# Kernel tuning notes

Hardware: AMD Instinct MI355X
Metric: run time of the kernel (lower is better)

Reference implementation:

```python
import jax, jax.numpy as jnp
import numpy as np

Z_DIM = 32
POLY_ORDER = 3
INCLUDE_BIAS = True

# Static index arrays replicating the nested-loop term ordering of the torch code.
_I2, _J2 = np.triu_indices(Z_DIM)  # pairs (i, j) with i <= j, row-major in i -> matches loop order
_TRIPLES = np.array([(i, j, k) for i in range(Z_DIM) for j in range(i, Z_DIM) for k in range(j, Z_DIM)], dtype=np.int32)
_TI, _TJ, _TK = _TRIPLES[:, 0], _TRIPLES[:, 1], _TRIPLES[:, 2]


def build_library(z):
    # z: [B, d] -> Theta: [B, n_terms], same column order as build_library_torch
    B = z.shape[0]
    terms = []
    if INCLUDE_BIAS:
        terms.append(jnp.ones((B, 1), dtype=z.dtype))
    terms.append(z)
    if POLY_ORDER >= 2:
        terms.append(z[:, _I2] * z[:, _J2])  # [B, C(d+1,2)] quadratic terms
    if POLY_ORDER >= 3:
        terms.append(z[:, _TI] * z[:, _TJ] * z[:, _TK])  # [B, C(d+2,3)] cubic terms
    return jnp.concatenate(terms, axis=1)


def setup_inputs() -> dict:
    key = jax.random.key(0)
    k1, k2 = jax.random.split(key)
    B = 65536
    n_terms = 6545  # 1 + 32 + 528 + 5984 for d=32, order=3, bias
    z = jax.random.normal(k1, (B, Z_DIM), dtype=jnp.float32)
    Xi = jax.random.normal(k2, (n_terms, Z_DIM), dtype=jnp.float32)
    Xi_mask = jnp.ones((n_terms, Z_DIM), dtype=jnp.float32)
    z_mean = jnp.zeros((1, Z_DIM), dtype=jnp.float32)
    z_std = jnp.ones((1, Z_DIM), dtype=jnp.float32)
    return {"z": z, "Xi": Xi, "Xi_mask": Xi_mask, "z_mean": z_mean, "z_std": z_std}


def reference(z, Xi, Xi_mask, z_mean, z_std):
    # NOTE: the original module computes z_norm = (z - z_mean) / z_std but
    # never uses it; Theta is built from the raw z. Reproduce exactly.
    Theta = build_library(z)            # [B, n_terms]
    Xi_eff = Xi * Xi_mask               # [n_terms, z_dim]
    dz_dt = Theta @ Xi_eff              # [B, z_dim]
    return dz_dt
```

## Files before the change

kernel.cpp:

```cpp
#include <hip/hip_runtime.h>


#define Z 32
#define ROWS 65536
#define NTILE (ROWS / 32)
#define NBLK (NTILE / 2)

#define NCHUNK 552
#define NGRAN (NCHUNK * 2)

typedef short short8 __attribute__((ext_vector_type(8)));
typedef float f32x16 __attribute__((ext_vector_type(16)));
typedef float float2v __attribute__((ext_vector_type(2)));

struct Sched {
    int nq[4];
    unsigned long long m2[NCHUNK];
    short rt[NGRAN * 8];
};

constexpr Sched make_sched() {
    Sched s{};
    short gi[NGRAN] = {}, gj[NGRAN] = {};
    char gt[NGRAN] = {}, gq[NGRAN] = {};
    int tidx[32][32] = {}, pidx[32] = {};
    {
        int n = 0;
        for (int a = 0; a < 32; ++a)
            for (int b = a; b < 32; ++b) { tidx[a][b] = n; n += 32 - b; }
        for (int i = 0; i < 32; ++i) pidx[i] = i * 32 - i * (i - 1) / 2;
    }
    int g = 0;
    for (int q = 0; q < 4; ++q) {
        int g0 = g;
        for (int b = 0; b < 32; ++b)
            if ((b >> 3) <= q)
                for (int a = 0; a <= b; ++a) { gi[g]=(short)a; gj[g]=(short)b; gt[g]=0; gq[g]=(char)q; ++g; }
        for (int b = 0; b < 32; ++b)
            if ((b >> 3) >= q) { gi[g]=(short)b; gj[g]=32; gt[g]=1; gq[g]=(char)q; ++g; }
        gi[g]=32; gj[g]=32; gt[g]=2; gq[g]=(char)q; ++g;
        while ((g - g0) & 7) { gi[g]=32; gj[g]=32; gt[g]=3; gq[g]=(char)q; ++g; }
        s.nq[q] = (g - g0) / 2;
    }
    for (int c = 0; c < NCHUNK; ++c) {
        unsigned lo = ((unsigned)gi[2*c]   * 4u) | (((unsigned)gj[2*c]   * 4u) << 16);
        unsigned hi = ((unsigned)gi[2*c+1] * 4u) | (((unsigned)gj[2*c+1] * 4u) << 16);
        s.m2[c] = (unsigned long long)lo | ((unsigned long long)hi << 32);
    }
    for (int gg = 0; gg < NGRAN; ++gg) {
        int i = gi[gg], j = gj[gg], ty = gt[gg], q = gq[gg];
        for (int jj = 0; jj < 8; ++jj) {
            int k = 8 * q + jj, row = -1;
            if (ty == 0)      { if (k >= j) row = 561 + tidx[i][j] + (k - j); }
            else if (ty == 1) { if (k <= i) row = 33 + pidx[k] + (i - k); }
            else if (ty == 2) { row = 1 + k; }
            s.rt[gg * 8 + jj] = (short)row;
        }
    }
    return s;
}
constexpr Sched S = make_sched();
static_assert(S.nq[0] == 36 && S.nq[1] == 84 && S.nq[2] == 160 && S.nq[3] == 272, "chunk counts");

__device__ __forceinline__ unsigned pack_bf16(float s0, float s1) {
#if __has_builtin(__builtin_amdgcn_cvt_pk_bf16_f32)
    return __builtin_bit_cast(unsigned, __builtin_amdgcn_cvt_pk_bf16_f32(s0, s1));
#else
    unsigned b0 = __builtin_bit_cast(unsigned, s0) + 0x8000u;
    unsigned b1 = __builtin_bit_cast(unsigned, s1) + 0x8000u;
    return __builtin_amdgcn_perm(b1, b0, 0x07060302u);
#endif
}

__global__ void sindy_prep(const float* __restrict__ Xi,
                           const float* __restrict__ Xi_mask,
                           uint2* __restrict__ Bp2, size_t ws_size) {
    int tid = blockIdx.x * blockDim.x + threadIdx.x;
    if (tid >= NGRAN * 64) return;
    int g = tid >> 6;
    int lane = tid & 63;
    int n = lane & 31, rep = lane >> 5;
    const short* rt = &S.rt[g * 8 + 4 * rep];
    unsigned v[4];
#pragma unroll
    for (int jj = 0; jj < 4; ++jj) {
        int row = rt[jj];
        float f = 0.0f;
        if (row >= 0) f = Xi[row * Z + n] * Xi_mask[row * Z + n];
        unsigned u = __builtin_bit_cast(unsigned, f);
        v[jj] = (u + 0x7FFFu + ((u >> 16) & 1u)) >> 16;
    }
    int c = g >> 1, h = g & 1;
    size_t idx = ((size_t)c * 64 + h * 32 + n) * 2 + rep;
    if ((idx + 1) * 8 <= ws_size)
        Bp2[idx] = uint2{v[0] | (v[1] << 16), v[2] | (v[3] << 16)};
}

template<int Q>
__device__ __forceinline__ void seg_run(int c0, int nG,
                                        const uint4* __restrict__ bpl,
                                        const float2v (&zr2)[16],
                                        const char* zbase, bool hi, f32x16& acc) {
    const uint4* p = bpl + (size_t)c0 * 64;
    uint4 cur0 = p[0], cur1 = p[64], cur2 = p[128], cur3 = p[192];
    int c = c0;
    auto body = [&](uint4 b0, uint4 b1, uint4 b2, uint4 b3) {
        const uint4 bb[4] = {b0, b1, b2, b3};
#pragma unroll
        for (int i = 0; i < 4; ++i) {
            unsigned long long m2 = S.m2[c + i];
            unsigned mw = hi ? (unsigned)(m2 >> 32) : (unsigned)m2;
            float zi = *(const float*)(zbase + (mw & 0xFFFFu));
            float zj = *(const float*)(zbase + (mw >> 16));
            float pp = zi * zj;
            float2v p2; p2.x = pp; p2.y = pp;
            union { unsigned u[4]; short8 s; } a;
#pragma unroll
            for (int r = 0; r < 4; ++r) {
                float2v t = p2 * zr2[4 * Q + r];
                a.u[r] = pack_bf16(t.x, t.y);
            }
            union { uint4 v; short8 s; } b; b.v = bb[i];
            acc = __builtin_amdgcn_mfma_f32_32x32x16_bf16(a.s, b.s, acc, 0, 0, 0);
        }
        c += 4;
    };
    for (int g = 0; g < nG - 1; ++g) {
        const uint4* pn = p + 256;
        uint4 n0 = pn[0], n1 = pn[64], n2 = pn[128], n3 = pn[192];
        body(cur0, cur1, cur2, cur3);
        cur0 = n0; cur1 = n1; cur2 = n2; cur3 = n3;
        p = pn;
    }
    body(cur0, cur1, cur2, cur3);
}

__global__ __launch_bounds__(256, 4) void sindy_mfma(const float* __restrict__ z,
                                                     const float* __restrict__ Xi,
                                                     const float* __restrict__ Xi_mask,
                                                     const uint4* __restrict__ Bp,
                                                     float* __restrict__ out) {
    const int lane = threadIdx.x & 63;
    const int w = threadIdx.x >> 6;
    const int tib = w >> 1;
    const int kh = w & 1;
    const int m = lane & 31;
    const int half = lane >> 5;
    const int tile = blockIdx.x * 2 + tib;
    const long R = (long)tile * 32;

    __shared__ float zs[2][32][33];
    __shared__ float cs[2][32][32];

    float2v zr2[16];
    const float4* z4 = (const float4*)(z + (R + m) * Z);
#pragma unroll
    for (int t = 0; t < 8; ++t) {
        float4 v = z4[t];
        zr2[2*t]   = float2v{v.x, v.y};
        zr2[2*t+1] = float2v{v.z, v.w};
    }
    if (kh == 0) {
#pragma unroll
        for (int t = 0; t < 8; ++t) {
            zs[tib][m][half * 16 + 2*t]     = zr2[half * 8 + t].x;
            zs[tib][m][half * 16 + 2*t + 1] = zr2[half * 8 + t].y;
        }
        if (half == 0) zs[tib][m][32] = 1.0f;
    }
    __syncthreads();

    f32x16 acc = {};
    const char* zbase = (const char*)&zs[tib][m][0];
    const uint4* bpl = Bp + lane;
    const bool hi = (half != 0);

    if (kh == 0) {
        seg_run<0>(  0,  9, bpl, zr2, zbase, hi, acc);
        seg_run<1>( 36, 21, bpl, zr2, zbase, hi, acc);
        seg_run<2>(120, 40, bpl, zr2, zbase, hi, acc);
    } else {
        seg_run<3>(280, 68, bpl, zr2, zbase, hi, acc);
#pragma unroll
        for (int r = 0; r < 16; ++r) {
            int row = (r & 3) + 8 * (r >> 2) + 4 * half;
            cs[tib][row][m] = acc[r];
        }
    }
    __syncthreads();

    if (kh == 0) {
        const float bias = Xi[m] * Xi_mask[m];
        float* orow = out + R * Z;
#pragma unroll
        for (int r = 0; r < 16; ++r) {
            int row = (r & 3) + 8 * (r >> 2) + 4 * half;
            orow[row * Z + m] = acc[r] + cs[tib][row][m] + bias;
        }
    }
}

extern "C" void kernel_launch(void* const* d_in, const int* in_sizes, int n_in,
                              void* d_out, int out_size, void* d_ws, size_t ws_size,
                              hipStream_t stream) {
    const float* z       = (const float*)d_in[0];
    const float* Xi      = (const float*)d_in[1];
    const float* Xi_mask = (const float*)d_in[2];
    float* out = (float*)d_out;
    uint4* Bp  = (uint4*)d_ws;

    int prep_threads = NGRAN * 64;
    sindy_prep<<<(prep_threads + 255) / 256, 256, 0, stream>>>(Xi, Xi_mask, (uint2*)d_ws, ws_size);
    sindy_mfma<<<NBLK, 256, 0, stream>>>(z, Xi, Xi_mask, Bp, out);
}
```

Measured before the change: 134.0 us.

## Rebalance K split across waves and software-pipeline schedule and z-product loads

Moves one chunk group from the first wave pair to the second so each handles 276 chunks instead of 280/272. The index schedule is copied into shared memory as per-granule words and prefetched two stages ahead. The z_i*z_j products for the next stage are computed before the current MFMAs issue, and the next B fragments are carried across segments instead of being reloaded. z values are now read from shared memory rather than kept as 32 registers, which lowers register pressure but adds LDS reads and a bit more LDS.

```diff
diff --git a/kernel.cpp b/kernel.cpp
--- a/kernel.cpp
+++ b/kernel.cpp
@@ -8,6 +8,7 @@
 
 #define NCHUNK 552
 #define NGRAN (NCHUNK * 2)
+#define KH_SPLIT 276
 
 typedef short short8 __attribute__((ext_vector_type(8)));
 typedef float f32x16 __attribute__((ext_vector_type(16)));
@@ -15,7 +16,7 @@
 
 struct Sched {
     int nq[4];
-    unsigned long long m2[NCHUNK];
+    unsigned mg[NGRAN];
     short rt[NGRAN * 8];
 };
 
@@ -42,12 +43,8 @@
         while ((g - g0) & 7) { gi[g]=32; gj[g]=32; gt[g]=3; gq[g]=(char)q; ++g; }
         s.nq[q] = (g - g0) / 2;
     }
-    for (int c = 0; c < NCHUNK; ++c) {
-        unsigned lo = ((unsigned)gi[2*c]   * 4u) | (((unsigned)gj[2*c]   * 4u) << 16);
-        unsigned hi = ((unsigned)gi[2*c+1] * 4u) | (((unsigned)gj[2*c+1] * 4u) << 16);
-        s.m2[c] = (unsigned long long)lo | ((unsigned long long)hi << 32);
-    }
     for (int gg = 0; gg < NGRAN; ++gg) {
+        s.mg[gg] = ((unsigned)gi[gg] * 4u) | (((unsigned)gj[gg] * 4u) << 16);
         int i = gi[gg], j = gj[gg], ty = gt[gg], q = gq[gg];
         for (int jj = 0; jj < 8; ++jj) {
             int k = 8 * q + jj, row = -1;
@@ -96,43 +93,72 @@
         Bp2[idx] = uint2{v[0] | (v[1] << 16), v[2] | (v[3] << 16)};
 }
 
-template<int Q>
-__device__ __forceinline__ void seg_run(int c0, int nG,
-                                        const uint4* __restrict__ bpl,
-                                        const float2v (&zr2)[16],
-                                        const char* zbase, bool hi, f32x16& acc) {
-    const uint4* p = bpl + (size_t)c0 * 64;
-    uint4 cur0 = p[0], cur1 = p[64], cur2 = p[128], cur3 = p[192];
-    int c = c0;
-    auto body = [&](uint4 b0, uint4 b1, uint4 b2, uint4 b3) {
-        const uint4 bb[4] = {b0, b1, b2, b3};
-#pragma unroll
-        for (int i = 0; i < 4; ++i) {
-            unsigned long long m2 = S.m2[c + i];
-            unsigned mw = hi ? (unsigned)(m2 >> 32) : (unsigned)m2;
-            float zi = *(const float*)(zbase + (mw & 0xFFFFu));
-            float zj = *(const float*)(zbase + (mw >> 16));
-            float pp = zi * zj;
-            float2v p2; p2.x = pp; p2.y = pp;
-            union { unsigned u[4]; short8 s; } a;
-#pragma unroll
-            for (int r = 0; r < 4; ++r) {
-                float2v t = p2 * zr2[4 * Q + r];
-                a.u[r] = pack_bf16(t.x, t.y);
-            }
-            union { uint4 v; short8 s; } b; b.v = bb[i];
-            acc = __builtin_amdgcn_mfma_f32_32x32x16_bf16(a.s, b.s, acc, 0, 0, 0);
-        }
-        c += 4;
+__device__ __forceinline__ float pprod(const char* zb, unsigned mw) {
+    float zi = *(const float*)(zb + (mw & 0xFFFFu));
+    float zj = *(const float*)(zb + (mw >> 16));
+    return zi * zj;
+}
+
+template<int Q, bool LAST>
+__device__ __forceinline__ void seg_run(int cbeg, int nSG,
+                                        const uint4*& p,
+                                        uint4& cur0, uint4& cur1, uint4& cur2, uint4& cur3,
+                                        const unsigned* __restrict__ mgh,
+                                        const char* __restrict__ zrowc,
+                                        f32x16& acc) {
+    const float* zrow = (const float*)zrowc;
+    float2v zq0, zq1, zq2, zq3;
+    zq0.x = zrow[8*Q+0]; zq0.y = zrow[8*Q+1];
+    zq1.x = zrow[8*Q+2]; zq1.y = zrow[8*Q+3];
+    zq2.x = zrow[8*Q+4]; zq2.y = zrow[8*Q+5];
+    zq3.x = zrow[8*Q+6]; zq3.y = zrow[8*Q+7];
+
+    auto chunk = [&](float pp, const uint4& bv) {
+        float2v p2; p2.x = pp; p2.y = pp;
+        union { unsigned u[4]; short8 sv; } a;
+        float2v t0 = p2 * zq0; a.u[0] = pack_bf16(t0.x, t0.y);
+        float2v t1 = p2 * zq1; a.u[1] = pack_bf16(t1.x, t1.y);
+        float2v t2 = p2 * zq2; a.u[2] = pack_bf16(t2.x, t2.y);
+        float2v t3 = p2 * zq3; a.u[3] = pack_bf16(t3.x, t3.y);
+        union { uint4 v; short8 sv; } b; b.v = bv;
+        acc = __builtin_amdgcn_mfma_f32_32x32x16_bf16(a.sv, b.sv, acc, 0, 0, 0);
     };
-    for (int g = 0; g < nG - 1; ++g) {
-        const uint4* pn = p + 256;
-        uint4 n0 = pn[0], n1 = pn[64], n2 = pn[128], n3 = pn[192];
-        body(cur0, cur1, cur2, cur3);
-        cur0 = n0; cur1 = n1; cur2 = n2; cur3 = n3;
-        p = pn;
-    }
-    body(cur0, cur1, cur2, cur3);
+
+    const unsigned* mg0 = mgh + 2 * cbeg;
+    float pC0 = pprod(zrowc, mg0[0]);
+    float pC1 = pprod(zrowc, mg0[2]);
+    float pC2 = pprod(zrowc, mg0[4]);
+    float pC3 = pprod(zrowc, mg0[6]);
+    unsigned w10 = 0, w11 = 0, w12 = 0, w13 = 0;
+    if (nSG > 1) {
+        const unsigned* mg1 = mgh + 2 * (cbeg + 4);
+        w10 = mg1[0]; w11 = mg1[2]; w12 = mg1[4]; w13 = mg1[6];
+    }
+
+    for (int s = 0; s < nSG; ++s) {
+        unsigned w20 = 0, w21 = 0, w22 = 0, w23 = 0;
+        if (s + 2 < nSG) {
+            const unsigned* mg2 = mgh + 2 * (cbeg + 4 * (s + 2));
+            w20 = mg2[0]; w21 = mg2[2]; w22 = mg2[4]; w23 = mg2[6];
+        }
+        float zi0=0,zj0=0,zi1=0,zj1=0,zi2=0,zj2=0,zi3=0,zj3=0;
+        bool more = (s + 1 < nSG);
+        if (more) {
+            zi0 = *(const float*)(zrowc + (w10 & 0xFFFFu)); zj0 = *(const float*)(zrowc + (w10 >> 16));
+            zi1 = *(const float*)(zrowc + (w11 & 0xFFFFu)); zj1 = *(const float*)(zrowc + (w11 >> 16));
+            zi2 = *(const float*)(zrowc + (w12 & 0xFFFFu)); zj2 = *(const float*)(zrowc + (w12 >> 16));
+            zi3 = *(const float*)(zrowc + (w13 & 0xFFFFu)); zj3 = *(const float*)(zrowc + (w13 >> 16));
+        }
+        bool pref = !(LAST && s == nSG - 1);
+        uint4 n0, n1, n2, n3;
+        if (pref) { n0 = p[256]; n1 = p[320]; n2 = p[384]; n3 = p[448]; }
+        chunk(pC0, cur0); chunk(pC1, cur1); chunk(pC2, cur2); chunk(pC3, cur3);
+        if (more) {
+            pC0 = zi0 * zj0; pC1 = zi1 * zj1; pC2 = zi2 * zj2; pC3 = zi3 * zj3;
+            w10 = w20; w11 = w21; w12 = w22; w13 = w23;
+        }
+        if (pref) { cur0 = n0; cur1 = n1; cur2 = n2; cur3 = n3; p += 256; }
+    }
 }
 
 __global__ __launch_bounds__(256, 4) void sindy_mfma(const float* __restrict__ z,
@@ -151,36 +177,38 @@
 
     __shared__ float zs[2][32][33];
     __shared__ float cs[2][32][32];
-
-    float2v zr2[16];
-    const float4* z4 = (const float4*)(z + (R + m) * Z);
-#pragma unroll
-    for (int t = 0; t < 8; ++t) {
-        float4 v = z4[t];
-        zr2[2*t]   = float2v{v.x, v.y};
-        zr2[2*t+1] = float2v{v.z, v.w};
-    }
+    __shared__ unsigned mg_sh[NGRAN];
+
+    for (int t = threadIdx.x; t < NGRAN; t += 256) mg_sh[t] = S.mg[t];
+
     if (kh == 0) {
+        const float4* z4 = (const float4*)(z + (R + m) * Z);
 #pragma unroll
         for (int t = 0; t < 8; ++t) {
-            zs[tib][m][half * 16 + 2*t]     = zr2[half * 8 + t].x;
-            zs[tib][m][half * 16 + 2*t + 1] = zr2[half * 8 + t].y;
+            float4 v = z4[t];
+            zs[tib][m][4*t+0] = v.x; zs[tib][m][4*t+1] = v.y;
+            zs[tib][m][4*t+2] = v.z; zs[tib][m][4*t+3] = v.w;
         }
         if (half == 0) zs[tib][m][32] = 1.0f;
     }
+
+    const int cbeg = kh ? KH_SPLIT : 0;
+    const uint4* p = Bp + lane + (size_t)cbeg * 64;
+    uint4 cur0 = p[0], cur1 = p[64], cur2 = p[128], cur3 = p[192];
+
     __syncthreads();
 
     f32x16 acc = {};
-    const char* zbase = (const char*)&zs[tib][m][0];
-    const uint4* bpl = Bp + lane;
-    const bool hi = (half != 0);
+    const char* zrowc = (const char*)&zs[tib][m][0];
+    const unsigned* mgh = mg_sh + half;
 
     if (kh == 0) {
-        seg_run<0>(  0,  9, bpl, zr2, zbase, hi, acc);
-        seg_run<1>( 36, 21, bpl, zr2, zbase, hi, acc);
-        seg_run<2>(120, 40, bpl, zr2, zbase, hi, acc);
+        seg_run<0, false>(  0,  9, p, cur0, cur1, cur2, cur3, mgh, zrowc, acc);
+        seg_run<1, false>( 36, 21, p, cur0, cur1, cur2, cur3, mgh, zrowc, acc);
+        seg_run<2, true >(120, 39, p, cur0, cur1, cur2, cur3, mgh, zrowc, acc);
     } else {
-        seg_run<3>(280, 68, bpl, zr2, zbase, hi, acc);
+        seg_run<2, false>(276,  1, p, cur0, cur1, cur2, cur3, mgh, zrowc, acc);
+        seg_run<3, true >(280, 68, p, cur0, cur1, cur2, cur3, mgh, zrowc, acc);
 #pragma unroll
         for (int r = 0; r < 16; ++r) {
             int row = (r & 3) + 8 * (r >> 2) + 4 * half;
```

Result: no change. 131.6 us (-1.8%).

## Split each 32-row tile's K-chunks across four waves with balanced ranges

Applied to the files above, without the earlier changes.

Each block now handles one 32-row tile, and its four waves split the 552 K-chunks into roughly equal ranges, where before two waves per tile split them unevenly. The partial accumulators are reduced through shared memory in two stages. z is stored transposed in LDS and re-read per segment, with software-pipelined index and B-operand prefetch, and launch bounds are raised to 8 blocks per CU. The prep kernel is restructured to stage values through shared memory for coalesced Xi reads. The aim is to balance MFMA work across waves and raise occupancy, at the cost of extra barriers and LDS traffic for the reduction.

```diff
diff --git a/kernel.cpp b/kernel.cpp
--- a/kernel.cpp
+++ b/kernel.cpp
@@ -3,8 +3,7 @@
 
 #define Z 32
 #define ROWS 65536
-#define NTILE (ROWS / 32)
-#define NBLK (NTILE / 2)
+#define NBLK (ROWS / 32)
 
 #define NCHUNK 552
 #define NGRAN (NCHUNK * 2)
@@ -15,7 +14,8 @@
 
 struct Sched {
     int nq[4];
-    unsigned long long m2[NCHUNK];
+    unsigned mlo[NCHUNK];
+    unsigned mhi[NCHUNK];
     short rt[NGRAN * 8];
 };
 
@@ -43,9 +43,8 @@
         s.nq[q] = (g - g0) / 2;
     }
     for (int c = 0; c < NCHUNK; ++c) {
-        unsigned lo = ((unsigned)gi[2*c]   * 4u) | (((unsigned)gj[2*c]   * 4u) << 16);
-        unsigned hi = ((unsigned)gi[2*c+1] * 4u) | (((unsigned)gj[2*c+1] * 4u) << 16);
-        s.m2[c] = (unsigned long long)lo | ((unsigned long long)hi << 32);
+        s.mlo[c] = ((unsigned)gi[2*c]   * 128u) | (((unsigned)gj[2*c]   * 128u) << 16);
+        s.mhi[c] = ((unsigned)gi[2*c+1] * 128u) | (((unsigned)gj[2*c+1] * 128u) << 16);
     }
     for (int gg = 0; gg < NGRAN; ++gg) {
         int i = gi[gg], j = gj[gg], ty = gt[gg], q = gq[gg];
@@ -75,127 +74,155 @@
 __global__ void sindy_prep(const float* __restrict__ Xi,
                            const float* __restrict__ Xi_mask,
                            uint2* __restrict__ Bp2, size_t ws_size) {
-    int tid = blockIdx.x * blockDim.x + threadIdx.x;
-    if (tid >= NGRAN * 64) return;
-    int g = tid >> 6;
-    int lane = tid & 63;
-    int n = lane & 31, rep = lane >> 5;
-    const short* rt = &S.rt[g * 8 + 4 * rep];
-    unsigned v[4];
-#pragma unroll
-    for (int jj = 0; jj < 4; ++jj) {
-        int row = rt[jj];
+    __shared__ unsigned short sh[8][32];
+    const int tid = threadIdx.x;
+    const int jj = tid >> 5, n = tid & 31;
+#pragma unroll
+    for (int pass = 0; pass < 4; ++pass) {
+        int g = blockIdx.x * 4 + pass;
+        int row = S.rt[g * 8 + jj];
         float f = 0.0f;
         if (row >= 0) f = Xi[row * Z + n] * Xi_mask[row * Z + n];
         unsigned u = __builtin_bit_cast(unsigned, f);
-        v[jj] = (u + 0x7FFFu + ((u >> 16) & 1u)) >> 16;
-    }
-    int c = g >> 1, h = g & 1;
-    size_t idx = ((size_t)c * 64 + h * 32 + n) * 2 + rep;
-    if ((idx + 1) * 8 <= ws_size)
-        Bp2[idx] = uint2{v[0] | (v[1] << 16), v[2] | (v[3] << 16)};
-}
-
-template<int Q>
-__device__ __forceinline__ void seg_run(int c0, int nG,
-                                        const uint4* __restrict__ bpl,
-                                        const float2v (&zr2)[16],
-                                        const char* zbase, bool hi, f32x16& acc) {
+        sh[jj][n] = (unsigned short)((u + 0x7FFFu + ((u >> 16) & 1u)) >> 16);
+        __syncthreads();
+        if (tid < 64) {
+            int n2 = tid & 31, rep = tid >> 5;
+            unsigned v0 = sh[4*rep+0][n2], v1 = sh[4*rep+1][n2];
+            unsigned v2 = sh[4*rep+2][n2], v3 = sh[4*rep+3][n2];
+            int c = g >> 1, h = g & 1;
+            size_t idx = ((size_t)c * 64 + h * 32 + n2) * 2 + rep;
+            if ((idx + 1) * 8 <= ws_size)
+                Bp2[idx] = uint2{v0 | (v1 << 16), v2 | (v3 << 16)};
+        }
+        __syncthreads();
+    }
+}
+
+template<int Q, bool LAST>
+__device__ __forceinline__ void seg(int c0, int cend,
+                                    const uint4* __restrict__ bpl,
+                                    const char* __restrict__ zb,
+                                    bool hi, f32x16& acc) {
+    float2v zqA, zqB, zqC, zqD;
+    zqA.x = *(const float*)(zb + (8*Q+0)*128); zqA.y = *(const float*)(zb + (8*Q+1)*128);
+    zqB.x = *(const float*)(zb + (8*Q+2)*128); zqB.y = *(const float*)(zb + (8*Q+3)*128);
+    zqC.x = *(const float*)(zb + (8*Q+4)*128); zqC.y = *(const float*)(zb + (8*Q+5)*128);
+    zqD.x = *(const float*)(zb + (8*Q+6)*128); zqD.y = *(const float*)(zb + (8*Q+7)*128);
+
+    auto chunk = [&](float pp, const uint4& bv) {
+        float2v p2; p2.x = pp; p2.y = pp;
+        union { unsigned u[4]; short8 sv; } a;
+        float2v t0 = p2 * zqA; a.u[0] = pack_bf16(t0.x, t0.y);
+        float2v t1 = p2 * zqB; a.u[1] = pack_bf16(t1.x, t1.y);
+        float2v t2 = p2 * zqC; a.u[2] = pack_bf16(t2.x, t2.y);
+        float2v t3 = p2 * zqD; a.u[3] = pack_bf16(t3.x, t3.y);
+        union { uint4 v; short8 sv; } b; b.v = bv;
+        acc = __builtin_amdgcn_mfma_f32_32x32x16_bf16(a.sv, b.sv, acc, 0, 0, 0);
+    };
+
     const uint4* p = bpl + (size_t)c0 * 64;
-    uint4 cur0 = p[0], cur1 = p[64], cur2 = p[128], cur3 = p[192];
-    int c = c0;
-    auto body = [&](uint4 b0, uint4 b1, uint4 b2, uint4 b3) {
-        const uint4 bb[4] = {b0, b1, b2, b3};
-#pragma unroll
-        for (int i = 0; i < 4; ++i) {
-            unsigned long long m2 = S.m2[c + i];
-            unsigned mw = hi ? (unsigned)(m2 >> 32) : (unsigned)m2;
-            float zi = *(const float*)(zbase + (mw & 0xFFFFu));
-            float zj = *(const float*)(zbase + (mw >> 16));
-            float pp = zi * zj;
-            float2v p2; p2.x = pp; p2.y = pp;
-            union { unsigned u[4]; short8 s; } a;
-#pragma unroll
-            for (int r = 0; r < 4; ++r) {
-                float2v t = p2 * zr2[4 * Q + r];
-                a.u[r] = pack_bf16(t.x, t.y);
-            }
-            union { uint4 v; short8 s; } b; b.v = bb[i];
-            acc = __builtin_amdgcn_mfma_f32_32x32x16_bf16(a.s, b.s, acc, 0, 0, 0);
-        }
-        c += 4;
-    };
-    for (int g = 0; g < nG - 1; ++g) {
-        const uint4* pn = p + 256;
-        uint4 n0 = pn[0], n1 = pn[64], n2 = pn[128], n3 = pn[192];
-        body(cur0, cur1, cur2, cur3);
-        cur0 = n0; cur1 = n1; cur2 = n2; cur3 = n3;
-        p = pn;
-    }
-    body(cur0, cur1, cur2, cur3);
-}
-
-__global__ __launch_bounds__(256, 4) void sindy_mfma(const float* __restrict__ z,
+    uint4 cur0 = p[0], cur1 = p[64];
+
+    unsigned mw0 = hi ? S.mhi[c0]     : S.mlo[c0];
+    unsigned mw1 = hi ? S.mhi[c0 + 1] : S.mlo[c0 + 1];
+    float pC0 = (*(const float*)(zb + (mw0 & 0xFFFFu))) * (*(const float*)(zb + (mw0 >> 16)));
+    float pC1 = (*(const float*)(zb + (mw1 & 0xFFFFu))) * (*(const float*)(zb + (mw1 >> 16)));
+    int c1 = (c0 + 2 < cend) ? c0 + 2 : c0;
+    unsigned mA0 = hi ? S.mhi[c1] : S.mlo[c1];
+    unsigned mA1 = hi ? S.mhi[c1 + 1] : S.mlo[c1 + 1];
+
+    for (int c = c0; c < cend; c += 2) {
+        bool more = (c + 2 < cend);
+        float zi0 = *(const float*)(zb + (mA0 & 0xFFFFu));
+        float zj0 = *(const float*)(zb + (mA0 >> 16));
+        float zi1 = *(const float*)(zb + (mA1 & 0xFFFFu));
+        float zj1 = *(const float*)(zb + (mA1 >> 16));
+        int cn = (c + 4 < cend) ? c + 4 : c;
+        unsigned mB0 = hi ? S.mhi[cn] : S.mlo[cn];
+        unsigned mB1 = hi ? S.mhi[cn + 1] : S.mlo[cn + 1];
+        int offn = (more || !LAST) ? 128 : 0;
+        uint4 n0 = p[offn], n1 = p[offn + 64];
+        chunk(pC0, cur0);
+        chunk(pC1, cur1);
+        pC0 = zi0 * zj0; pC1 = zi1 * zj1;
+        mA0 = mB0; mA1 = mB1;
+        cur0 = n0; cur1 = n1;
+        p += offn;
+    }
+}
+
+__global__ __launch_bounds__(256, 8) void sindy_mfma(const float* __restrict__ z,
                                                      const float* __restrict__ Xi,
                                                      const float* __restrict__ Xi_mask,
                                                      const uint4* __restrict__ Bp,
                                                      float* __restrict__ out) {
     const int lane = threadIdx.x & 63;
-    const int w = threadIdx.x >> 6;
-    const int tib = w >> 1;
-    const int kh = w & 1;
+    const int kh = threadIdx.x >> 6;
     const int m = lane & 31;
     const int half = lane >> 5;
-    const int tile = blockIdx.x * 2 + tib;
-    const long R = (long)tile * 32;
-
-    __shared__ float zs[2][32][33];
+    const long R = (long)blockIdx.x * 32;
+
+    __shared__ float zs[33][32];
     __shared__ float cs[2][32][32];
 
-    float2v zr2[16];
-    const float4* z4 = (const float4*)(z + (R + m) * Z);
-#pragma unroll
-    for (int t = 0; t < 8; ++t) {
-        float4 v = z4[t];
-        zr2[2*t]   = float2v{v.x, v.y};
-        zr2[2*t+1] = float2v{v.z, v.w};
-    }
-    if (kh == 0) {
-#pragma unroll
-        for (int t = 0; t < 8; ++t) {
-            zs[tib][m][half * 16 + 2*t]     = zr2[half * 8 + t].x;
-            zs[tib][m][half * 16 + 2*t + 1] = zr2[half * 8 + t].y;
-        }
-        if (half == 0) zs[tib][m][32] = 1.0f;
+    {
+        const float4* z4 = (const float4*)(z + (R + m) * Z + 8 * kh);
+        float4 v0 = z4[0], v1 = z4[1];
+        zs[8*kh+0][m] = v0.x; zs[8*kh+1][m] = v0.y; zs[8*kh+2][m] = v0.z; zs[8*kh+3][m] = v0.w;
+        zs[8*kh+4][m] = v1.x; zs[8*kh+5][m] = v1.y; zs[8*kh+6][m] = v1.z; zs[8*kh+7][m] = v1.w;
+        if (kh == 0 && half == 0) zs[32][m] = 1.0f;
     }
     __syncthreads();
 
     f32x16 acc = {};
-    const char* zbase = (const char*)&zs[tib][m][0];
+    const char* zb = (const char*)&zs[0][0] + 4 * m;
     const uint4* bpl = Bp + lane;
     const bool hi = (half != 0);
 
     if (kh == 0) {
-        seg_run<0>(  0,  9, bpl, zr2, zbase, hi, acc);
-        seg_run<1>( 36, 21, bpl, zr2, zbase, hi, acc);
-        seg_run<2>(120, 40, bpl, zr2, zbase, hi, acc);
+        seg<0, false>(  0,  36, bpl, zb, hi, acc);
+        seg<1, false>( 36, 120, bpl, zb, hi, acc);
+        seg<2, true >(120, 136, bpl, zb, hi, acc);
+    } else if (kh == 1) {
+        seg<2, true >(136, 276, bpl, zb, hi, acc);
+    } else if (kh == 2) {
+        seg<2, false>(276, 280, bpl, zb, hi, acc);
+        seg<3, true >(280, 416, bpl, zb, hi, acc);
     } else {
-        seg_run<3>(280, 68, bpl, zr2, zbase, hi, acc);
-#pragma unroll
-        for (int r = 0; r < 16; ++r) {
-            int row = (r & 3) + 8 * (r >> 2) + 4 * half;
-            cs[tib][row][m] = acc[r];
+        seg<3, true >(416, 552, bpl, zb, hi, acc);
+    }
+
+    if (kh == 1 || kh == 3) {
+        float (*dst)[32] = cs[kh >> 1];
+#pragma unroll
+        for (int r = 0; r < 16; ++r) {
+            int row = (r & 3) + 8 * (r >> 2) + 4 * half;
+            dst[row][m] = acc[r];
         }
     }
     __syncthreads();
-
+    if (kh == 0) {
+#pragma unroll
+        for (int r = 0; r < 16; ++r) {
+            int row = (r & 3) + 8 * (r >> 2) + 4 * half;
+            acc[r] += cs[0][row][m];
+        }
+    } else if (kh == 2) {
+#pragma unroll
+        for (int r = 0; r < 16; ++r) {
+            int row = (r & 3) + 8 * (r >> 2) + 4 * half;
+            cs[1][row][m] += acc[r];
+        }
+    }
+    __syncthreads();
     if (kh == 0) {
         const float bias = Xi[m] * Xi_mask[m];
         float* orow = out + R * Z;
 #pragma unroll
         for (int r = 0; r < 16; ++r) {
             int row = (r & 3) + 8 * (r >> 2) + 4 * half;
-            orow[row * Z + m] = acc[r] + cs[tib][row][m] + bias;
+            orow[row * Z + m] = acc[r] + cs[1][row][m] + bias;
         }
     }
 }
@@ -209,7 +236,6 @@
     float* out = (float*)d_out;
     uint4* Bp  = (uint4*)d_ws;
 
-    int prep_threads = NGRAN * 64;
-    sindy_prep<<<(prep_threads + 255) / 256, 256, 0, stream>>>(Xi, Xi_mask, (uint2*)d_ws, ws_size);
+    sindy_prep<<<NGRAN / 4, 256, 0, stream>>>(Xi, Xi_mask, (uint2*)d_ws, ws_size);
     sindy_mfma<<<NBLK, 256, 0, stream>>>(z, Xi, Xi_mask, Bp, out);
 }
```

After: 137.7 us. 2.7% more time.

## Fully unroll K loop at compile time with register-resident z and balanced K split

Applied to the files above, without the earlier changes.

Replaces the per-chunk LDS lookups of z_i*z_j with a compile-time recursive template that fully unrolls all 552 chunks, so every index becomes a constant and operands are read directly from registers. The K range is now split evenly between the two waves at chunk 276 instead of by quadrant segment, which balances the work. It also removes the LDS z staging and one barrier, and restructures the prep kernel so each block transposes through shared memory. The price is very large code size, heavy compile time, and possible instruction-cache pressure or register spills.

```diff
diff --git a/kernel.cpp b/kernel.cpp
--- a/kernel.cpp
+++ b/kernel.cpp
@@ -3,26 +3,25 @@
 
 #define Z 32
 #define ROWS 65536
-#define NTILE (ROWS / 32)
-#define NBLK (NTILE / 2)
+#define NBLK (ROWS / 64)
 
 #define NCHUNK 552
 #define NGRAN (NCHUNK * 2)
+#define KSPLIT 276
 
 typedef short short8 __attribute__((ext_vector_type(8)));
 typedef float f32x16 __attribute__((ext_vector_type(16)));
 typedef float float2v __attribute__((ext_vector_type(2)));
 
 struct Sched {
+    short gi[NGRAN], gj[NGRAN];
+    char gq[NGRAN];
+    short rt[NGRAN * 8];
     int nq[4];
-    unsigned long long m2[NCHUNK];
-    short rt[NGRAN * 8];
 };
 
 constexpr Sched make_sched() {
     Sched s{};
-    short gi[NGRAN] = {}, gj[NGRAN] = {};
-    char gt[NGRAN] = {}, gq[NGRAN] = {};
     int tidx[32][32] = {}, pidx[32] = {};
     {
         int n = 0;
@@ -35,26 +34,38 @@
         int g0 = g;
         for (int b = 0; b < 32; ++b)
             if ((b >> 3) <= q)
-                for (int a = 0; a <= b; ++a) { gi[g]=(short)a; gj[g]=(short)b; gt[g]=0; gq[g]=(char)q; ++g; }
-        for (int b = 0; b < 32; ++b)
-            if ((b >> 3) >= q) { gi[g]=(short)b; gj[g]=32; gt[g]=1; gq[g]=(char)q; ++g; }
-        gi[g]=32; gj[g]=32; gt[g]=2; gq[g]=(char)q; ++g;
-        while ((g - g0) & 7) { gi[g]=32; gj[g]=32; gt[g]=3; gq[g]=(char)q; ++g; }
+                for (int a = 0; a <= b; ++a) { s.gi[g]=(short)a; s.gj[g]=(short)b; s.gq[g]=(char)q; ++g; }
+        for (int b = 0; b < 32; ++b)
+            if ((b >> 3) >= q) { s.gi[g]=(short)b; s.gj[g]=32; s.gq[g]=(char)q; ++g; }
+        s.gi[g]=32; s.gj[g]=32; s.gq[g]=(char)q; ++g;
+        while ((g - g0) & 7) { s.gi[g]=32; s.gj[g]=32; s.gq[g]=(char)q; ++g; }
         s.nq[q] = (g - g0) / 2;
     }
-    for (int c = 0; c < NCHUNK; ++c) {
-        unsigned lo = ((unsigned)gi[2*c]   * 4u) | (((unsigned)gj[2*c]   * 4u) << 16);
-        unsigned hi = ((unsigned)gi[2*c+1] * 4u) | (((unsigned)gj[2*c+1] * 4u) << 16);
-        s.m2[c] = (unsigned long long)lo | ((unsigned long long)hi << 32);
-    }
-    for (int gg = 0; gg < NGRAN; ++gg) {
-        int i = gi[gg], j = gj[gg], ty = gt[gg], q = gq[gg];
-        for (int jj = 0; jj < 8; ++jj) {
-            int k = 8 * q + jj, row = -1;
-            if (ty == 0)      { if (k >= j) row = 561 + tidx[i][j] + (k - j); }
-            else if (ty == 1) { if (k <= i) row = 33 + pidx[k] + (i - k); }
-            else if (ty == 2) { row = 1 + k; }
-            s.rt[gg * 8 + jj] = (short)row;
+    g = 0;
+    for (int q = 0; q < 4; ++q) {
+        int g0 = g;
+        for (int b = 0; b < 32; ++b)
+            if ((b >> 3) <= q)
+                for (int a = 0; a <= b; ++a) {
+                    for (int jj = 0; jj < 8; ++jj) {
+                        int k = 8 * q + jj;
+                        s.rt[g*8+jj] = (short)((k >= b) ? 561 + tidx[a][b] + (k - b) : -1);
+                    }
+                    ++g;
+                }
+        for (int b = 0; b < 32; ++b)
+            if ((b >> 3) >= q) {
+                for (int jj = 0; jj < 8; ++jj) {
+                    int k = 8 * q + jj;
+                    s.rt[g*8+jj] = (short)((k <= b) ? 33 + pidx[k] + (b - k) : -1);
+                }
+                ++g;
+            }
+        for (int jj = 0; jj < 8; ++jj) s.rt[g*8+jj] = (short)(1 + 8*q + jj);
+        ++g;
+        while ((g - g0) & 7) {
+            for (int jj = 0; jj < 8; ++jj) s.rt[g*8+jj] = -1;
+            ++g;
         }
     }
     return s;
@@ -75,64 +86,70 @@
 __global__ void sindy_prep(const float* __restrict__ Xi,
                            const float* __restrict__ Xi_mask,
                            uint2* __restrict__ Bp2, size_t ws_size) {
-    int tid = blockIdx.x * blockDim.x + threadIdx.x;
-    if (tid >= NGRAN * 64) return;
-    int g = tid >> 6;
-    int lane = tid & 63;
-    int n = lane & 31, rep = lane >> 5;
-    const short* rt = &S.rt[g * 8 + 4 * rep];
-    unsigned v[4];
-#pragma unroll
-    for (int jj = 0; jj < 4; ++jj) {
-        int row = rt[jj];
+    __shared__ unsigned short sh[8][32];
+    const int tid = threadIdx.x;
+    const int jj = tid >> 5, n = tid & 31;
+#pragma unroll
+    for (int pass = 0; pass < 4; ++pass) {
+        int g = blockIdx.x * 4 + pass;
+        int row = S.rt[g * 8 + jj];
         float f = 0.0f;
         if (row >= 0) f = Xi[row * Z + n] * Xi_mask[row * Z + n];
         unsigned u = __builtin_bit_cast(unsigned, f);
-        v[jj] = (u + 0x7FFFu + ((u >> 16) & 1u)) >> 16;
-    }
-    int c = g >> 1, h = g & 1;
-    size_t idx = ((size_t)c * 64 + h * 32 + n) * 2 + rep;
-    if ((idx + 1) * 8 <= ws_size)
-        Bp2[idx] = uint2{v[0] | (v[1] << 16), v[2] | (v[3] << 16)};
-}
-
-template<int Q>
-__device__ __forceinline__ void seg_run(int c0, int nG,
-                                        const uint4* __restrict__ bpl,
-                                        const float2v (&zr2)[16],
-                                        const char* zbase, bool hi, f32x16& acc) {
-    const uint4* p = bpl + (size_t)c0 * 64;
-    uint4 cur0 = p[0], cur1 = p[64], cur2 = p[128], cur3 = p[192];
-    int c = c0;
-    auto body = [&](uint4 b0, uint4 b1, uint4 b2, uint4 b3) {
-        const uint4 bb[4] = {b0, b1, b2, b3};
-#pragma unroll
-        for (int i = 0; i < 4; ++i) {
-            unsigned long long m2 = S.m2[c + i];
-            unsigned mw = hi ? (unsigned)(m2 >> 32) : (unsigned)m2;
-            float zi = *(const float*)(zbase + (mw & 0xFFFFu));
-            float zj = *(const float*)(zbase + (mw >> 16));
-            float pp = zi * zj;
-            float2v p2; p2.x = pp; p2.y = pp;
-            union { unsigned u[4]; short8 s; } a;
-#pragma unroll
-            for (int r = 0; r < 4; ++r) {
-                float2v t = p2 * zr2[4 * Q + r];
-                a.u[r] = pack_bf16(t.x, t.y);
-            }
-            union { uint4 v; short8 s; } b; b.v = bb[i];
-            acc = __builtin_amdgcn_mfma_f32_32x32x16_bf16(a.s, b.s, acc, 0, 0, 0);
-        }
-        c += 4;
-    };
-    for (int g = 0; g < nG - 1; ++g) {
-        const uint4* pn = p + 256;
-        uint4 n0 = pn[0], n1 = pn[64], n2 = pn[128], n3 = pn[192];
-        body(cur0, cur1, cur2, cur3);
-        cur0 = n0; cur1 = n1; cur2 = n2; cur3 = n3;
-        p = pn;
-    }
-    body(cur0, cur1, cur2, cur3);
+        sh[jj][n] = (unsigned short)((u + 0x7FFFu + ((u >> 16) & 1u)) >> 16);
+        __syncthreads();
+        if (tid < 64) {
+            int n2 = tid & 31, rep = tid >> 5;
+            unsigned v0 = sh[4*rep+0][n2], v1 = sh[4*rep+1][n2];
+            unsigned v2 = sh[4*rep+2][n2], v3 = sh[4*rep+3][n2];
+            int c = g >> 1, h = g & 1;
+            size_t idx = ((size_t)c * 64 + h * 32 + n2) * 2 + rep;
+            if ((idx + 1) * 8 <= ws_size)
+                Bp2[idx] = uint2{v0 | (v1 << 16), v2 | (v3 << 16)};
+        }
+        __syncthreads();
+    }
+}
+
+struct ZReg { float2v v[17]; };
+
+template<int C0, int C1>
+__device__ __forceinline__ void kloop(const ZReg& Zr, bool hi,
+                                      const uint4* __restrict__ bpl,
+                                      uint4& b0, uint4& b1, uint4& b2, uint4& b3,
+                                      f32x16& acc) {
+    if constexpr (C1 - C0 > 1) {
+        constexpr int M = C0 + (C1 - C0) / 2;
+        kloop<C0, M>(Zr, hi, bpl, b0, b1, b2, b3, acc);
+        kloop<M, C1>(Zr, hi, bpl, b0, b1, b2, b3, acc);
+    } else {
+        constexpr int C = C0;
+        constexpr int i0 = S.gi[2*C],   j0 = S.gj[2*C];
+        constexpr int i1 = S.gi[2*C+1], j1 = S.gj[2*C+1];
+        constexpr int q  = S.gq[2*C];
+        float p0 = Zr.v[i0/2][i0%2] * Zr.v[j0/2][j0%2];
+        float p1 = Zr.v[i1/2][i1%2] * Zr.v[j1/2][j1%2];
+        float pp = hi ? p1 : p0;
+        float2v p2 = {pp, pp};
+        union { unsigned u[4]; short8 sv; } a;
+        float2v t0 = p2 * Zr.v[4*q+0]; a.u[0] = pack_bf16(t0.x, t0.y);
+        float2v t1 = p2 * Zr.v[4*q+1]; a.u[1] = pack_bf16(t1.x, t1.y);
+        float2v t2 = p2 * Zr.v[4*q+2]; a.u[2] = pack_bf16(t2.x, t2.y);
+        float2v t3 = p2 * Zr.v[4*q+3]; a.u[3] = pack_bf16(t3.x, t3.y);
+        union { uint4 v; short8 sv; } b;
+        if constexpr (C % 4 == 0) b.v = b0;
+        else if constexpr (C % 4 == 1) b.v = b1;
+        else if constexpr (C % 4 == 2) b.v = b2;
+        else b.v = b3;
+        acc = __builtin_amdgcn_mfma_f32_32x32x16_bf16(a.sv, b.sv, acc, 0, 0, 0);
+        if constexpr (C + 4 < NCHUNK) {
+            uint4 nb = bpl[(size_t)(C + 4) * 64];
+            if constexpr (C % 4 == 0) b0 = nb;
+            else if constexpr (C % 4 == 1) b1 = nb;
+            else if constexpr (C % 4 == 2) b2 = nb;
+            else b3 = nb;
+        }
+    }
 }
 
 __global__ __launch_bounds__(256, 4) void sindy_mfma(const float* __restrict__ z,
@@ -146,41 +163,34 @@
     const int kh = w & 1;
     const int m = lane & 31;
     const int half = lane >> 5;
-    const int tile = blockIdx.x * 2 + tib;
-    const long R = (long)tile * 32;
-
-    __shared__ float zs[2][32][33];
+    const long R = (long)blockIdx.x * 64 + tib * 32;
+
     __shared__ float cs[2][32][32];
 
-    float2v zr2[16];
+    ZReg Zr;
     const float4* z4 = (const float4*)(z + (R + m) * Z);
 #pragma unroll
     for (int t = 0; t < 8; ++t) {
         float4 v = z4[t];
-        zr2[2*t]   = float2v{v.x, v.y};
-        zr2[2*t+1] = float2v{v.z, v.w};
-    }
+        Zr.v[2*t]   = float2v{v.x, v.y};
+        Zr.v[2*t+1] = float2v{v.z, v.w};
+    }
+    Zr.v[16] = float2v{1.0f, 0.0f};
+
+    const bool hi = (half != 0);
+    const uint4* bpl = Bp + lane;
+    f32x16 acc = {};
+
     if (kh == 0) {
-#pragma unroll
-        for (int t = 0; t < 8; ++t) {
-            zs[tib][m][half * 16 + 2*t]     = zr2[half * 8 + t].x;
-            zs[tib][m][half * 16 + 2*t + 1] = zr2[half * 8 + t].y;
-        }
-        if (half == 0) zs[tib][m][32] = 1.0f;
-    }
-    __syncthreads();
-
-    f32x16 acc = {};
-    const char* zbase = (const char*)&zs[tib][m][0];
-    const uint4* bpl = Bp + lane;
-    const bool hi = (half != 0);
-
-    if (kh == 0) {
-        seg_run<0>(  0,  9, bpl, zr2, zbase, hi, acc);
-        seg_run<1>( 36, 21, bpl, zr2, zbase, hi, acc);
-        seg_run<2>(120, 40, bpl, zr2, zbase, hi, acc);
+        uint4 b0 = bpl[0], b1 = bpl[64], b2 = bpl[128], b3 = bpl[192];
+        kloop<0, KSPLIT>(Zr, hi, bpl, b0, b1, b2, b3, acc);
     } else {
-        seg_run<3>(280, 68, bpl, zr2, zbase, hi, acc);
+        uint4 b0 = bpl[(size_t)KSPLIT * 64],       b1 = bpl[(size_t)(KSPLIT+1) * 64],
+              b2 = bpl[(size_t)(KSPLIT+2) * 64],   b3 = bpl[(size_t)(KSPLIT+3) * 64];
+        kloop<KSPLIT, NCHUNK>(Zr, hi, bpl, b0, b1, b2, b3, acc);
+    }
+
+    if (kh == 1) {
 #pragma unroll
         for (int r = 0; r < 16; ++r) {
             int row = (r & 3) + 8 * (r >> 2) + 4 * half;
@@ -188,7 +198,6 @@
         }
     }
     __syncthreads();
-
     if (kh == 0) {
         const float bias = Xi[m] * Xi_mask[m];
         float* orow = out + R * Z;
@@ -209,7 +218,6 @@
     float* out = (float*)d_out;
     uint4* Bp  = (uint4*)d_ws;
 
-    int prep_threads = NGRAN * 64;
-    sindy_prep<<<(prep_threads + 255) / 256, 256, 0, stream>>>(Xi, Xi_mask, (uint2*)d_ws, ws_size);
+    sindy_prep<<<NGRAN / 4, 256, 0, stream>>>(Xi, Xi_mask, (uint2*)d_ws, ws_size);
     sindy_mfma<<<NBLK, 256, 0, stream>>>(z, Xi, Xi_mask, Bp, out);
 }
```

Result: slower. 151.3 us (+12.9%).
